# Kernel optimization log

Measured on AMD Instinct MI355X. Metric: run time of the kernel, lower is better.

Reference implementation:

```python
import jax, jax.numpy as jnp
import numpy as np

N0, N1, N2 = 200000, 50000, 10000
D_IN, D_PROMPT, D_HID, D_OUT = 128, 64, 256, 2
E0, E1 = 800000, 160000


def _glorot(key, shape):
    fan_in, fan_out = shape[0], shape[1]
    lim = np.sqrt(6.0 / (fan_in + fan_out))
    return jax.random.uniform(key, shape, jnp.float32, -lim, lim)


def setup_inputs() -> dict:
    key = jax.random.key(0)
    ks = jax.random.split(key, 20)
    inp = {
        "features": jax.random.normal(ks[0], (N0, D_IN), jnp.float32),
        "membership_mask": jax.random.randint(ks[1], (N0,), 0, 2) > 0,
        "src0": jax.random.randint(ks[2], (E0,), 0, N0),
        "dst0": jax.random.randint(ks[3], (E0,), 0, N1),
        "src1": jax.random.randint(ks[4], (E1,), 0, N1),
        "dst1": jax.random.randint(ks[5], (E1,), 0, N2),
        "output_nodes_indices": jax.random.randint(ks[6], (N2,), 0, N2),
        # prompt MLPs
        "w_pin": _glorot(ks[7], (D_IN, D_PROMPT)),
        "b_pin": jnp.zeros((D_PROMPT,), jnp.float32),
        "w_pout": _glorot(ks[8], (D_IN, D_PROMPT)),
        "b_pout": jnp.zeros((D_PROMPT,), jnp.float32),
        # SAGEConv layer 0: (D_IN+D_PROMPT) -> D_HID
        "w_self0": _glorot(ks[9], (D_IN + D_PROMPT, D_HID)),
        "w_neigh0": _glorot(ks[10], (D_IN + D_PROMPT, D_HID)),
        "b0": jnp.zeros((D_HID,), jnp.float32),
        # SAGEConv layer 1: D_HID -> D_HID
        "w_self1": _glorot(ks[11], (D_HID, D_HID)),
        "w_neigh1": _glorot(ks[12], (D_HID, D_HID)),
        "b1": jnp.zeros((D_HID,), jnp.float32),
        # classifier
        "w_cls": _glorot(ks[13], (D_HID, D_OUT)),
        "b_cls": jnp.zeros((D_OUT,), jnp.float32),
    }
    return inp


def _sage_mean(h, src, dst, n_dst, w_self, w_neigh, b):
    # mean-aggregate src features into dst buckets (zero-degree -> 0, DGL semantics)
    agg = jax.ops.segment_sum(h[src], dst, num_segments=n_dst)
    deg = jax.ops.segment_sum(jnp.ones((src.shape[0],), h.dtype), dst, num_segments=n_dst)
    agg = agg / jnp.maximum(deg, 1.0)[:, None]
    return h[:n_dst] @ w_self + agg @ w_neigh + b


def reference(features, membership_mask, src0, dst0, src1, dst1, output_nodes_indices,
              w_pin, b_pin, w_pout, b_pout,
              w_self0, w_neigh0, b0, w_self1, w_neigh1, b1, w_cls, b_cls):
    p_in = jax.nn.relu(features @ w_pin + b_pin)
    p_out = jax.nn.relu(features @ w_pout + b_pout)
    sel = jnp.where(membership_mask[:, None], p_in, p_out)
    h = jnp.concatenate([features, sel], axis=1)          # [N0, D_IN+D_PROMPT]
    h = jax.nn.relu(_sage_mean(h, src0, dst0, N1, w_self0, w_neigh0, b0))  # [N1, D_HID]
    h = _sage_mean(h, src1, dst1, N2, w_self1, w_neigh1, b1)               # [N2, D_HID]
    logits = h @ w_cls + b_cls                             # [N2, D_OUT]
    return logits
```

## Files before the change

### kernel.cpp

```cpp
#include <hip/hip_runtime.h>


#define N0v 200000
#define N1v 50000
#define N2v 10000
#define E0v 800000
#define E1v 160000
#define TB0 49
#define TB1 10
#define TBL (TB0 + TB1)

using u16 = unsigned short;
typedef __attribute__((ext_vector_type(8))) short short8;
typedef __attribute__((ext_vector_type(4))) float f32x4;

__device__ __forceinline__ float b2f(u16 u) {
    union { unsigned int i; float f; } v; v.i = ((unsigned int)u) << 16; return v.f;
}
__device__ __forceinline__ u16 f2b(float f) {
    union { float f; unsigned int i; } v; v.f = f;
    return (u16)((v.i + 0x7fffu + ((v.i >> 16) & 1u)) >> 16);
}
__device__ __forceinline__ void split2(float f, u16& h, u16& l) {
    h = f2b(f);
    l = f2b(f - b2f(h));
}

__global__ void k_prep(const unsigned* mask, int* flag,
                       const float* w_pin, const float* w_pout, u16* WTph, u16* WTpl,
                       const float* ws0, const float* wn0, u16* WT0h, u16* WT0l,
                       const float* ws1, const float* wn1, u16* WT1h, u16* WT1l,
                       const float* bc, float* outp,
                       const int* __restrict__ dst0, const int* __restrict__ dst1,
                       int* cnt0, int* cnt1) {
    const int R0 = 50000;
    const int R1 = R0 + 128 * 128;
    const int R2 = R1 + 256 * 384;
    const int R3 = R2 + 256 * 512;
    const int R4 = R3 + 2 * N2v;
    const int R5 = R4 + E0v;
    const int R6 = R5 + E1v;
    for (int i = blockIdx.x * blockDim.x + threadIdx.x; i < R6;
         i += gridDim.x * blockDim.x) {
        if (i < R0) {
            if (mask[i] > 1u) atomicOr(flag, 1);
        } else if (i < R1) {
            int j = i - R0, n = j >> 7, k = j & 127;
            float f = (n < 64) ? w_pin[k * 64 + n] : w_pout[k * 64 + (n - 64)];
            split2(f, WTph[j], WTpl[j]);
        } else if (i < R2) {
            int j = i - R1, n = j / 384, k = j % 384;
            float f = (k < 192) ? ws0[k * 256 + n] : wn0[(k - 192) * 256 + n];
            split2(f, WT0h[j], WT0l[j]);
        } else if (i < R3) {
            int j = i - R2, n = j >> 9, k = j & 511;
            float f = (k < 256) ? ws1[k * 256 + n] : wn1[(k - 256) * 256 + n];
            split2(f, WT1h[j], WT1l[j]);
        } else if (i < R4) {
            int j = i - R3;
            outp[j] = bc[j & 1];
        } else if (i < R5) {
            atomicAdd(&cnt0[dst0[i - R4]], 1);
        } else {
            atomicAdd(&cnt1[dst1[i - R5]], 1);
        }
    }
}

__global__ __launch_bounds__(256) void k_scan_a(const int* __restrict__ cnt0,
                                                int* __restrict__ off0,
                                                const int* __restrict__ cnt1,
                                                int* __restrict__ off1,
                                                int* __restrict__ tsum) {
    __shared__ int sd[256];
    const int t = threadIdx.x;
    const int blk = blockIdx.x;
    const int g1 = (blk >= TB0);
    const int b = g1 ? blk - TB0 : blk;
    const int n = g1 ? N2v : N1v;
    const int* cnt = g1 ? cnt1 : cnt0;
    int* off = g1 ? off1 : off0;
    const int i0 = b * 1024 + t * 4;
    int c[4] = {0, 0, 0, 0};
    if (i0 + 3 < n) {
        *(int4*)c = *(const int4*)&cnt[i0];
    } else {
        for (int j = 0; j < 4; j++) if (i0 + j < n) c[j] = cnt[i0 + j];
    }
    int s = c[0] + c[1] + c[2] + c[3];
    sd[t] = s;
    __syncthreads();
#pragma unroll
    for (int d = 1; d < 256; d <<= 1) {
        int v = (t >= d) ? sd[t - d] : 0;
        __syncthreads();
        sd[t] += v;
        __syncthreads();
    }
    int run = sd[t] - s;
    int o4[4];
#pragma unroll
    for (int j = 0; j < 4; j++) { o4[j] = run; run += c[j]; }
    if (i0 + 3 < n) *(int4*)&off[i0] = *(const int4*)o4;
    else for (int j = 0; j < 4; j++) if (i0 + j < n) off[i0 + j] = o4[j];
    if (t == 255) tsum[blk] = sd[255];
}

__global__ __launch_bounds__(256) void k_scan_c(int* __restrict__ off0,
                                                int* __restrict__ off1,
                                                const int* __restrict__ tsum) {
    __shared__ int lbase;
    const int t = threadIdx.x;
    const int blk = blockIdx.x;
    const int g1 = (blk >= TB0);
    const int b = g1 ? blk - TB0 : blk;
    const int n = g1 ? N2v : N1v;
    int* off = g1 ? off1 : off0;
    if (t < 64) {
        int v = (t < TBL) ? tsum[t] : 0;
        int incl = v;
#pragma unroll
        for (int d = 1; d < 64; d <<= 1) {
            int u = __shfl_up(incl, d);
            if (t >= d) incl += u;
        }
        int total0 = __shfl(incl, TB0 - 1);
        if (t == blk) lbase = (incl - v) - (g1 ? total0 : 0);
    }
    __syncthreads();
    const int base = lbase;
    const int i0 = b * 1024 + t * 4;
    if (i0 + 3 < n) {
        int4 v = *(int4*)&off[i0];
        v.x += base; v.y += base; v.z += base; v.w += base;
        *(int4*)&off[i0] = v;
    } else {
        for (int j = 0; j < 4; j++) if (i0 + j < n) off[i0 + j] += base;
    }
    if (blk == 0 && t == 0) { off0[N1v] = E0v; off1[N2v] = E1v; }
}

__global__ void k_scatter2(const int* __restrict__ src0, const int* __restrict__ dst0,
                           const int* __restrict__ off0, int* cur0, int* ei0,
                           const int* __restrict__ src1, const int* __restrict__ dst1,
                           const int* __restrict__ off1, int* cur1, int* ei1) {
    for (int i = blockIdx.x * blockDim.x + threadIdx.x; i < E0v + E1v;
         i += gridDim.x * blockDim.x) {
        if (i < E0v) {
            int d = dst0[i];
            ei0[off0[d] + atomicAdd(&cur0[d], 1)] = src0[i];
        } else {
            int d = dst1[i - E0v];
            ei1[off1[d] + atomicAdd(&cur1[d], 1)] = src1[i - E0v];
        }
    }
}

__global__ __launch_bounds__(256, 3) void k_gemm_p(
    const float* __restrict__ A, const u16* __restrict__ Bh, const u16* __restrict__ Bl,
    const float* __restrict__ b_pin, const float* __restrict__ b_pout,
    const void* maskp, const int* __restrict__ flag, u16* __restrict__ G) {
    __shared__ __align__(16) u16 LA[8704];
    const int t = threadIdx.x;
    const int bm = blockIdx.x;
    const int lane = t & 63, w = t >> 6;
    const int m = lane & 15, q = lane >> 4;
    const int r0 = bm * 64;
    const int colbase = w * 32;

    short8 bf[2][4][2];
#pragma unroll
    for (int nt = 0; nt < 2; nt++)
#pragma unroll
        for (int k0 = 0; k0 < 4; k0++) {
            size_t b = (size_t)(colbase + nt * 16 + m) * 128 + k0 * 32 + q * 8;
            bf[nt][k0][0] = *(const short8*)&Bh[b];
            bf[nt][k0][1] = *(const short8*)&Bl[b];
        }

    {
        const int r15 = t >> 4, ch = t & 15;
        const int k0 = ch >> 2, q2 = ch & 3;
#pragma unroll
        for (int p = 0; p < 4; p++) {
            const int row = r0 + r15 + 16 * p;
            const float* ap = &A[(size_t)row * 128 + ch * 8];
            float4 v0 = *(const float4*)ap, v1 = *(const float4*)(ap + 4);
            u16 h8[8];
            h8[0] = f2b(v0.x); h8[1] = f2b(v0.y); h8[2] = f2b(v0.z); h8[3] = f2b(v0.w);
            h8[4] = f2b(v1.x); h8[5] = f2b(v1.y); h8[6] = f2b(v1.z); h8[7] = f2b(v1.w);
            *(uint4*)&G[(size_t)row * 192 + ch * 8] = *(const uint4*)h8;
            *(uint4*)&LA[((p * 4 + k0) * 66 + 16 * q2 + r15) * 8] = *(const uint4*)h8;
        }
    }
    __syncthreads();

    f32x4 acc[4][2] = {};
#pragma unroll
    for (int mi = 0; mi < 4; mi++) {
#pragma unroll
        for (int k0 = 0; k0 < 4; k0++) {
            short8 af = *(const short8*)&LA[((mi * 4 + k0) * 66 + lane) * 8];
#pragma unroll
            for (int nt = 0; nt < 2; nt++) {
                acc[mi][nt] = __builtin_amdgcn_mfma_f32_16x16x32_bf16(af, bf[nt][k0][0], acc[mi][nt], 0, 0, 0);
                acc[mi][nt] = __builtin_amdgcn_mfma_f32_16x16x32_bf16(af, bf[nt][k0][1], acc[mi][nt], 0, 0, 0);
            }
        }
    }

    float bv[2];
#pragma unroll
    for (int nt = 0; nt < 2; nt++) {
        int col = colbase + nt * 16 + m;
        bv[nt] = (col < 64) ? b_pin[col] : b_pout[col - 64];
    }
    __syncthreads();
#pragma unroll
    for (int mi = 0; mi < 4; mi++)
#pragma unroll
        for (int nt = 0; nt < 2; nt++)
#pragma unroll
            for (int r = 0; r < 4; r++) {
                float v = acc[mi][nt][r] + bv[nt];
                v = v > 0.f ? v : 0.f;
                LA[(mi * 16 + q * 4 + r) * 136 + colbase + nt * 16 + m] = f2b(v);
            }
    __syncthreads();
    const int fl = *flag;
    {
        const int c8 = t & 7;
#pragma unroll
        for (int pass = 0; pass < 2; pass++) {
            const int rt = pass * 32 + (t >> 3);
            const int row = r0 + rt;
            bool mk = fl ? (((const unsigned char*)maskp)[row] != 0)
                         : (((const int*)maskp)[row] != 0);
            const int src = mk ? 0 : 64;
            *(uint4*)&G[(size_t)row * 192 + 128 + c8 * 8] =
                *(const uint4*)&LA[rt * 136 + src + c8 * 8];
        }
    }
}

template <int MODE, int KT, int KE0, int MT>
__global__ __launch_bounds__(256, 3) void k_g(
    const u16* __restrict__ A0, int s0, const u16* __restrict__ A1, int s1,
    const u16* __restrict__ Bh, const u16* __restrict__ Bl,
    const float* __restrict__ bias,
    u16* __restrict__ CH, float* __restrict__ outp, const float* __restrict__ wc,
    int M) {
    constexpr int MI = MT / 16;
    __shared__ __align__(16) u16 LA[MI * KT * 66 * 8];
    const int t = threadIdx.x;
    const int bm = blockIdx.x >> 1, bn = blockIdx.x & 1;
    const int lane = t & 63, w = t >> 6;
    const int m = lane & 15, q = lane >> 4;
    const int r0 = bm * MT;
    const int colbase = bn * 128 + w * 32;
    const int K = KT * 32;

    {
        constexpr int TPR = 256 / MT;
        constexpr int SPT = KT / TPR;
        const int rr = t / TPR, sub = t & (TPR - 1);
        int arow = r0 + rr; if (arow >= M) arow = M - 1;
        const int mi = rr >> 4, r15 = rr & 15;
#pragma unroll
        for (int s = 0; s < SPT; s++) {
            const int kc = sub * SPT + s;
#pragma unroll
            for (int q2 = 0; q2 < 4; q2++) {
                const int c = kc * 32 + q2 * 8;
                uint4 v = (c < KE0 * 32)
                              ? *(const uint4*)&A0[(size_t)arow * s0 + c]
                              : *(const uint4*)&A1[(size_t)arow * s1 + (c - KE0 * 32)];
                *(uint4*)&LA[((mi * KT + kc) * 66 + 16 * q2 + r15) * 8] = v;
            }
        }
    }
    __syncthreads();

    f32x4 acc[MI][2] = {};
#pragma unroll 1
    for (int kb = 0; kb < KT; kb += 4) {
        short8 bf[2][4][2];
#pragma unroll
        for (int nt = 0; nt < 2; nt++)
#pragma unroll
            for (int k0 = 0; k0 < 4; k0++) {
                size_t b = (size_t)(colbase + nt * 16 + m) * K + (kb + k0) * 32 + q * 8;
                bf[nt][k0][0] = *(const short8*)&Bh[b];
                bf[nt][k0][1] = *(const short8*)&Bl[b];
            }
#pragma unroll
        for (int mi = 0; mi < MI; mi++) {
#pragma unroll
            for (int k0 = 0; k0 < 4; k0++) {
                short8 af = *(const short8*)&LA[((mi * KT + kb + k0) * 66 + lane) * 8];
#pragma unroll
                for (int nt = 0; nt < 2; nt++) {
                    acc[mi][nt] = __builtin_amdgcn_mfma_f32_16x16x32_bf16(af, bf[nt][k0][0], acc[mi][nt], 0, 0, 0);
                    acc[mi][nt] = __builtin_amdgcn_mfma_f32_16x16x32_bf16(af, bf[nt][k0][1], acc[mi][nt], 0, 0, 0);
                }
            }
        }
    }

    if (MODE == 1) {
        float bv[2];
#pragma unroll
        for (int nt = 0; nt < 2; nt++) bv[nt] = bias[colbase + nt * 16 + m];
        __syncthreads();
#pragma unroll
        for (int mi = 0; mi < MI; mi++)
#pragma unroll
            for (int nt = 0; nt < 2; nt++)
#pragma unroll
                for (int r = 0; r < 4; r++) {
                    float v = acc[mi][nt][r] + bv[nt];
                    v = v > 0.f ? v : 0.f;
                    LA[(mi * 16 + q * 4 + r) * 136 + w * 32 + nt * 16 + m] = f2b(v);
                }
        __syncthreads();
        const int c16 = t & 15;
#pragma unroll
        for (int pass = 0; pass < MT / 16; pass++) {
            const int rt = pass * 16 + (t >> 4);
            const int row = r0 + rt;
            if (row < M) {
                *(uint4*)&CH[(size_t)row * 256 + bn * 128 + c16 * 8] =
                    *(const uint4*)&LA[rt * 136 + c16 * 8];
            }
        }
    } else {
        const int ca = colbase + m, cb = colbase + 16 + m;
        const float bva = bias[ca], bvb = bias[cb];
        const float w0a = wc[ca * 2], w1a = wc[ca * 2 + 1];
        const float w0b = wc[cb * 2], w1b = wc[cb * 2 + 1];
#pragma unroll
        for (int mi = 0; mi < MI; mi++) {
#pragma unroll
            for (int r = 0; r < 4; r++) {
                int row = r0 + mi * 16 + q * 4 + r;
                float va = acc[mi][0][r] + bva;
                float vb = acc[mi][1][r] + bvb;
                float p0 = va * w0a + vb * w0b;
                float p1 = va * w1a + vb * w1b;
#pragma unroll
                for (int s = 1; s < 16; s <<= 1) {
                    p0 += __shfl_xor(p0, s);
                    p1 += __shfl_xor(p1, s);
                }
                if (m == 0 && row < M) {
                    atomicAdd(&outp[row * 2], p0);
                    atomicAdd(&outp[row * 2 + 1], p1);
                }
            }
        }
    }
}

__global__ void k_agg0(const u16* __restrict__ G, const int* __restrict__ off,
                       const int* __restrict__ eidx, u16* __restrict__ aggH) {
    int wid = (blockIdx.x * blockDim.x + threadIdx.x) >> 6;
    int lane = threadIdx.x & 63;
    if (wid >= N1v) return;
    int b = off[wid], e = off[wid + 1];
    float f0 = 0.f, f1 = 0.f, p0 = 0.f;
    for (int base = b; base < e; base += 64) {
        int li = base + lane;
        int idx = eidx[li < e ? li : (e - 1)];
        int nch = e - base; if (nch > 64) nch = 64;
        int j = 0;
        for (; j + 4 <= nch; j += 4) {
            int sa = __shfl(idx, j), sb = __shfl(idx, j + 1);
            int sc = __shfl(idx, j + 2), sd = __shfl(idx, j + 3);
            const u16* ra = &G[(size_t)sa * 192];
            const u16* rb = &G[(size_t)sb * 192];
            const u16* rc = &G[(size_t)sc * 192];
            const u16* rd = &G[(size_t)sd * 192];
            unsigned fa = *(const unsigned*)&ra[2 * lane];
            unsigned fb = *(const unsigned*)&rb[2 * lane];
            unsigned fc = *(const unsigned*)&rc[2 * lane];
            unsigned fd = *(const unsigned*)&rd[2 * lane];
            u16 pa = ra[128 + lane], pb = rb[128 + lane];
            u16 pc = rc[128 + lane], pd = rd[128 + lane];
            f0 += b2f((u16)fa) + b2f((u16)fb) + b2f((u16)fc) + b2f((u16)fd);
            f1 += b2f((u16)(fa >> 16)) + b2f((u16)(fb >> 16)) +
                  b2f((u16)(fc >> 16)) + b2f((u16)(fd >> 16));
            p0 += b2f(pa) + b2f(pb) + b2f(pc) + b2f(pd);
        }
        for (; j < nch; j++) {
            int s = __shfl(idx, j);
            const u16* row = &G[(size_t)s * 192];
            unsigned fv = *(const unsigned*)&row[2 * lane];
            f0 += b2f((u16)fv);
            f1 += b2f((u16)(fv >> 16));
            p0 += b2f(row[128 + lane]);
        }
    }
    int deg = e - b;
    float inv = 1.0f / (float)(deg > 1 ? deg : 1);
    size_t rb2 = (size_t)wid * 192;
    *(unsigned*)&aggH[rb2 + 2 * lane] =
        (unsigned)f2b(f0 * inv) | ((unsigned)f2b(f1 * inv) << 16);
    aggH[rb2 + 128 + lane] = f2b(p0 * inv);
}

__global__ void k_agg1(const u16* __restrict__ h1H, const int* __restrict__ off,
                       const int* __restrict__ eidx, u16* __restrict__ aggH) {
    int wid = (blockIdx.x * blockDim.x + threadIdx.x) >> 6;
    int lane = threadIdx.x & 63;
    if (wid >= N2v) return;
    int b = off[wid], e = off[wid + 1];
    float a0 = 0.f, a1 = 0.f, a2 = 0.f, a3 = 0.f;
    for (int base = b; base < e; base += 64) {
        int li = base + lane;
        int idx = eidx[li < e ? li : (e - 1)];
        int nch = e - base; if (nch > 64) nch = 64;
        int j = 0;
        for (; j + 4 <= nch; j += 4) {
            int sa = __shfl(idx, j), sb = __shfl(idx, j + 1);
            int sc = __shfl(idx, j + 2), sd = __shfl(idx, j + 3);
            const u16* ra = &h1H[(size_t)sa * 256];
            const u16* rb = &h1H[(size_t)sb * 256];
            const u16* rc = &h1H[(size_t)sc * 256];
            const u16* rd = &h1H[(size_t)sd * 256];
            unsigned va0 = *(const unsigned*)&ra[2 * lane];
            unsigned vb0 = *(const unsigned*)&rb[2 * lane];
            unsigned vc0 = *(const unsigned*)&rc[2 * lane];
            unsigned vd0 = *(const unsigned*)&rd[2 * lane];
            unsigned va1 = *(const unsigned*)&ra[128 + 2 * lane];
            unsigned vb1 = *(const unsigned*)&rb[128 + 2 * lane];
            unsigned vc1 = *(const unsigned*)&rc[128 + 2 * lane];
            unsigned vd1 = *(const unsigned*)&rd[128 + 2 * lane];
            a0 += b2f((u16)va0) + b2f((u16)vb0) + b2f((u16)vc0) + b2f((u16)vd0);
            a1 += b2f((u16)(va0 >> 16)) + b2f((u16)(vb0 >> 16)) +
                  b2f((u16)(vc0 >> 16)) + b2f((u16)(vd0 >> 16));
            a2 += b2f((u16)va1) + b2f((u16)vb1) + b2f((u16)vc1) + b2f((u16)vd1);
            a3 += b2f((u16)(va1 >> 16)) + b2f((u16)(vb1 >> 16)) +
                  b2f((u16)(vc1 >> 16)) + b2f((u16)(vd1 >> 16));
        }
        for (; j < nch; j++) {
            int s = __shfl(idx, j);
            const u16* row = &h1H[(size_t)s * 256];
            unsigned v0 = *(const unsigned*)&row[2 * lane];
            unsigned v1 = *(const unsigned*)&row[128 + 2 * lane];
            a0 += b2f((u16)v0); a1 += b2f((u16)(v0 >> 16));
            a2 += b2f((u16)v1); a3 += b2f((u16)(v1 >> 16));
        }
    }
    int deg = e - b;
    float inv = 1.0f / (float)(deg > 1 ? deg : 1);
    size_t rb2 = (size_t)wid * 256;
    *(unsigned*)&aggH[rb2 + 2 * lane] =
        (unsigned)f2b(a0 * inv) | ((unsigned)f2b(a1 * inv) << 16);
    *(unsigned*)&aggH[rb2 + 128 + 2 * lane] =
        (unsigned)f2b(a2 * inv) | ((unsigned)f2b(a3 * inv) << 16);
}

extern "C" void kernel_launch(void* const* d_in, const int* in_sizes, int n_in,
                              void* d_out, int out_size, void* d_ws, size_t ws_size,
                              hipStream_t stream) {
    const float* features = (const float*)d_in[0];
    const void* maskp     = d_in[1];
    const int* src0       = (const int*)d_in[2];
    const int* dst0       = (const int*)d_in[3];
    const int* src1       = (const int*)d_in[4];
    const int* dst1       = (const int*)d_in[5];
    const float* w_pin    = (const float*)d_in[7];
    const float* b_pin    = (const float*)d_in[8];
    const float* w_pout   = (const float*)d_in[9];
    const float* b_pout   = (const float*)d_in[10];
    const float* w_self0  = (const float*)d_in[11];
    const float* w_neigh0 = (const float*)d_in[12];
    const float* b0       = (const float*)d_in[13];
    const float* w_self1  = (const float*)d_in[14];
    const float* w_neigh1 = (const float*)d_in[15];
    const float* b1       = (const float*)d_in[16];
    const float* w_cls    = (const float*)d_in[17];
    const float* b_cls    = (const float*)d_in[18];
    float* out = (float*)d_out;
    (void)in_sizes; (void)n_in; (void)out_size; (void)ws_size;

    char* ws = (char*)d_ws;
    size_t o = 0;
    auto alloc = [&](size_t bytes) { size_t r = o; o += (bytes + 255) & ~(size_t)255; return r; };
    size_t o_flag = alloc(4);
    size_t o_cnt0 = alloc(N1v * 4);
    size_t o_cur0 = alloc(N1v * 4);
    size_t o_cnt1 = alloc(N2v * 4);
    size_t o_cur1 = alloc(N2v * 4);
    size_t zero_end = o;
    size_t o_G    = alloc((size_t)N0v * 192 * 2);
    size_t o_aggH = alloc((size_t)N1v * 192 * 2);
    size_t o_h1H  = alloc((size_t)N1v * 256 * 2);
    size_t o_ag1H = alloc((size_t)N2v * 256 * 2);
    size_t o_wtph = alloc(128 * 128 * 2), o_wtpl = alloc(128 * 128 * 2);
    size_t o_wt0h = alloc(256 * 384 * 2), o_wt0l = alloc(256 * 384 * 2);
    size_t o_wt1h = alloc(256 * 512 * 2), o_wt1l = alloc(256 * 512 * 2);
    size_t o_off0 = alloc((N1v + 1) * 4);
    size_t o_off1 = alloc((N2v + 1) * 4);
    size_t o_ei0  = alloc((size_t)E0v * 4);
    size_t o_ei1  = alloc((size_t)E1v * 4);
    size_t o_tsum = alloc(TBL * 4);

    int* flag = (int*)(ws + o_flag);
    int* cnt0 = (int*)(ws + o_cnt0);
    int* cur0 = (int*)(ws + o_cur0);
    int* cnt1 = (int*)(ws + o_cnt1);
    int* cur1 = (int*)(ws + o_cur1);
    u16* G     = (u16*)(ws + o_G);
    u16* aggH  = (u16*)(ws + o_aggH);
    u16* h1H   = (u16*)(ws + o_h1H);
    u16* ag1H  = (u16*)(ws + o_ag1H);
    u16* WTph = (u16*)(ws + o_wtph);
    u16* WTpl = (u16*)(ws + o_wtpl);
    u16* WT0h = (u16*)(ws + o_wt0h);
    u16* WT0l = (u16*)(ws + o_wt0l);
    u16* WT1h = (u16*)(ws + o_wt1h);
    u16* WT1l = (u16*)(ws + o_wt1l);
    int* off0 = (int*)(ws + o_off0);
    int* off1 = (int*)(ws + o_off1);
    int* ei0  = (int*)(ws + o_ei0);
    int* ei1  = (int*)(ws + o_ei1);
    int* tsum = (int*)(ws + o_tsum);

    hipMemsetAsync(ws + o_flag, 0, zero_end - o_flag, stream);

    k_prep<<<1024, 256, 0, stream>>>((const unsigned*)maskp, flag,
                                     w_pin, w_pout, WTph, WTpl,
                                     w_self0, w_neigh0, WT0h, WT0l,
                                     w_self1, w_neigh1, WT1h, WT1l,
                                     b_cls, out, dst0, dst1, cnt0, cnt1);

    k_scan_a<<<TBL, 256, 0, stream>>>(cnt0, off0, cnt1, off1, tsum);
    k_scan_c<<<TBL, 256, 0, stream>>>(off0, off1, tsum);

    k_scatter2<<<1024, 256, 0, stream>>>(src0, dst0, off0, cur0, ei0,
                                         src1, dst1, off1, cur1, ei1);

    k_gemm_p<<<N0v / 64, 256, 0, stream>>>(features, WTph, WTpl,
                                           b_pin, b_pout, maskp, flag, G);

    k_agg0<<<(N1v + 3) / 4, 256, 0, stream>>>(G, off0, ei0, aggH);

    k_g<1, 12, 6, 64><<<((N1v + 63) / 64) * 2, 256, 0, stream>>>(
        G, 192, aggH, 192, WT0h, WT0l, b0, h1H, nullptr, nullptr, N1v);

    k_agg1<<<(N2v + 3) / 4, 256, 0, stream>>>(h1H, off1, ei1, ag1H);

    k_g<3, 16, 8, 32><<<((N2v + 31) / 32) * 2, 256, 0, stream>>>(
        h1H, 256, ag1H, 256, WT1h, WT1l, b1, nullptr, out, w_cls, N2v);
}
```

Measured before the change: 445.2 us.

## Record edge ranks during counting, partition scatter, and stream B fragments in GEMMs

The counting pass now stores the return value of each atomicAdd as the edge's rank within its destination bucket. The scatter uses that rank directly instead of a second round of atomics on cursor arrays. The scatter also splits its grid into 8 destination partitions, so each block re-reads its edge chunk but only writes edges whose destination falls in its partition, to localise writes. Both GEMM kernels load B fragments one k-step at a time (prefetched in k_gemm_p) instead of holding all of them in registers, mask loads are hoisted, and k_gemm_p's launch-bounds occupancy goes from 3 to 4; the cost is extra rank buffers and redundant index reads in the scatter.

Measured after the change: 422.0 us. 1.05x faster.

```diff
diff --git a/kernel.cpp b/kernel.cpp
--- a/kernel.cpp
+++ b/kernel.cpp
@@ -32,7 +32,7 @@
                        const float* ws1, const float* wn1, u16* WT1h, u16* WT1l,
                        const float* bc, float* outp,
                        const int* __restrict__ dst0, const int* __restrict__ dst1,
-                       int* cnt0, int* cnt1) {
+                       int* cnt0, int* cnt1, int* rk0, int* rk1) {
     const int R0 = 50000;
     const int R1 = R0 + 128 * 128;
     const int R2 = R1 + 256 * 384;
@@ -60,9 +60,11 @@
             int j = i - R3;
             outp[j] = bc[j & 1];
         } else if (i < R5) {
-            atomicAdd(&cnt0[dst0[i - R4]], 1);
+            int e = i - R4;
+            rk0[e] = atomicAdd(&cnt0[dst0[e]], 1);
         } else {
-            atomicAdd(&cnt1[dst1[i - R5]], 1);
+            int e = i - R5;
+            rk1[e] = atomicAdd(&cnt1[dst1[e]], 1);
         }
     }
 }
@@ -140,23 +142,33 @@
     if (blk == 0 && t == 0) { off0[N1v] = E0v; off1[N2v] = E1v; }
 }
 
-__global__ void k_scatter2(const int* __restrict__ src0, const int* __restrict__ dst0,
-                           const int* __restrict__ off0, int* cur0, int* ei0,
-                           const int* __restrict__ src1, const int* __restrict__ dst1,
-                           const int* __restrict__ off1, int* cur1, int* ei1) {
-    for (int i = blockIdx.x * blockDim.x + threadIdx.x; i < E0v + E1v;
-         i += gridDim.x * blockDim.x) {
-        if (i < E0v) {
+__global__ __launch_bounds__(256) void k_scatter2(
+    const int* __restrict__ src0, const int* __restrict__ dst0,
+    const int* __restrict__ off0, const int* __restrict__ rk0, int* __restrict__ ei0,
+    const int* __restrict__ src1, const int* __restrict__ dst1,
+    const int* __restrict__ off1, const int* __restrict__ rk1, int* __restrict__ ei1) {
+    const int part = blockIdx.x & 7;
+    const int chunk = blockIdx.x >> 3;
+    const int nch = gridDim.x >> 3;
+    {
+        const int per = (E0v + nch - 1) / nch;
+        const int i1 = min((chunk + 1) * per, E0v);
+        for (int i = chunk * per + (int)threadIdx.x; i < i1; i += 256) {
             int d = dst0[i];
-            ei0[off0[d] + atomicAdd(&cur0[d], 1)] = src0[i];
-        } else {
-            int d = dst1[i - E0v];
-            ei1[off1[d] + atomicAdd(&cur1[d], 1)] = src1[i - E0v];
-        }
-    }
-}
-
-__global__ __launch_bounds__(256, 3) void k_gemm_p(
+            if (d / 6250 == part) ei0[off0[d] + rk0[i]] = src0[i];
+        }
+    }
+    {
+        const int per = (E1v + nch - 1) / nch;
+        const int i1 = min((chunk + 1) * per, E1v);
+        for (int i = chunk * per + (int)threadIdx.x; i < i1; i += 256) {
+            int d = dst1[i];
+            if (d / 1250 == part) ei1[off1[d] + rk1[i]] = src1[i];
+        }
+    }
+}
+
+__global__ __launch_bounds__(256, 4) void k_gemm_p(
     const float* __restrict__ A, const u16* __restrict__ Bh, const u16* __restrict__ Bl,
     const float* __restrict__ b_pin, const float* __restrict__ b_pout,
     const void* maskp, const int* __restrict__ flag, u16* __restrict__ G) {
@@ -168,15 +180,25 @@
     const int r0 = bm * 64;
     const int colbase = w * 32;
 
-    short8 bf[2][4][2];
-#pragma unroll
-    for (int nt = 0; nt < 2; nt++)
-#pragma unroll
-        for (int k0 = 0; k0 < 4; k0++) {
-            size_t b = (size_t)(colbase + nt * 16 + m) * 128 + k0 * 32 + q * 8;
-            bf[nt][k0][0] = *(const short8*)&Bh[b];
-            bf[nt][k0][1] = *(const short8*)&Bl[b];
-        }
+    const int fl = *flag;
+    bool mk0, mk1;
+    {
+        const int ra = r0 + (t >> 3), rb = ra + 32;
+        if (fl) {
+            mk0 = ((const unsigned char*)maskp)[ra] != 0;
+            mk1 = ((const unsigned char*)maskp)[rb] != 0;
+        } else {
+            mk0 = ((const int*)maskp)[ra] != 0;
+            mk1 = ((const int*)maskp)[rb] != 0;
+        }
+    }
+
+    const size_t ba = (size_t)(colbase + m) * 128 + q * 8;
+    const size_t bb = (size_t)(colbase + 16 + m) * 128 + q * 8;
+    short8 nb0h = *(const short8*)&Bh[ba];
+    short8 nb0l = *(const short8*)&Bl[ba];
+    short8 nb1h = *(const short8*)&Bh[bb];
+    short8 nb1l = *(const short8*)&Bl[bb];
 
     {
         const int r15 = t >> 4, ch = t & 15;
@@ -197,15 +219,21 @@
 
     f32x4 acc[4][2] = {};
 #pragma unroll
-    for (int mi = 0; mi < 4; mi++) {
-#pragma unroll
-        for (int k0 = 0; k0 < 4; k0++) {
+    for (int k0 = 0; k0 < 4; k0++) {
+        short8 b0h = nb0h, b0l = nb0l, b1h = nb1h, b1l = nb1l;
+        if (k0 < 3) {
+            nb0h = *(const short8*)&Bh[ba + (k0 + 1) * 32];
+            nb0l = *(const short8*)&Bl[ba + (k0 + 1) * 32];
+            nb1h = *(const short8*)&Bh[bb + (k0 + 1) * 32];
+            nb1l = *(const short8*)&Bl[bb + (k0 + 1) * 32];
+        }
+#pragma unroll
+        for (int mi = 0; mi < 4; mi++) {
             short8 af = *(const short8*)&LA[((mi * 4 + k0) * 66 + lane) * 8];
-#pragma unroll
-            for (int nt = 0; nt < 2; nt++) {
-                acc[mi][nt] = __builtin_amdgcn_mfma_f32_16x16x32_bf16(af, bf[nt][k0][0], acc[mi][nt], 0, 0, 0);
-                acc[mi][nt] = __builtin_amdgcn_mfma_f32_16x16x32_bf16(af, bf[nt][k0][1], acc[mi][nt], 0, 0, 0);
-            }
+            acc[mi][0] = __builtin_amdgcn_mfma_f32_16x16x32_bf16(af, b0h, acc[mi][0], 0, 0, 0);
+            acc[mi][0] = __builtin_amdgcn_mfma_f32_16x16x32_bf16(af, b0l, acc[mi][0], 0, 0, 0);
+            acc[mi][1] = __builtin_amdgcn_mfma_f32_16x16x32_bf16(af, b1h, acc[mi][1], 0, 0, 0);
+            acc[mi][1] = __builtin_amdgcn_mfma_f32_16x16x32_bf16(af, b1l, acc[mi][1], 0, 0, 0);
         }
     }
 
@@ -227,19 +255,13 @@
                 LA[(mi * 16 + q * 4 + r) * 136 + colbase + nt * 16 + m] = f2b(v);
             }
     __syncthreads();
-    const int fl = *flag;
     {
         const int c8 = t & 7;
-#pragma unroll
-        for (int pass = 0; pass < 2; pass++) {
-            const int rt = pass * 32 + (t >> 3);
-            const int row = r0 + rt;
-            bool mk = fl ? (((const unsigned char*)maskp)[row] != 0)
-                         : (((const int*)maskp)[row] != 0);
-            const int src = mk ? 0 : 64;
-            *(uint4*)&G[(size_t)row * 192 + 128 + c8 * 8] =
-                *(const uint4*)&LA[rt * 136 + src + c8 * 8];
-        }
+        const int rt = t >> 3;
+        *(uint4*)&G[(size_t)(r0 + rt) * 192 + 128 + c8 * 8] =
+            *(const uint4*)&LA[rt * 136 + (mk0 ? 0 : 64) + c8 * 8];
+        *(uint4*)&G[(size_t)(r0 + 32 + rt) * 192 + 128 + c8 * 8] =
+            *(const uint4*)&LA[(32 + rt) * 136 + (mk1 ? 0 : 64) + c8 * 8];
     }
 }
 
@@ -281,28 +303,26 @@
     }
     __syncthreads();
 
+    const size_t ba = (size_t)(colbase + m) * K + q * 8;
+    const size_t bb = (size_t)(colbase + 16 + m) * K + q * 8;
+
     f32x4 acc[MI][2] = {};
 #pragma unroll 1
     for (int kb = 0; kb < KT; kb += 4) {
-        short8 bf[2][4][2];
-#pragma unroll
-        for (int nt = 0; nt < 2; nt++)
-#pragma unroll
-            for (int k0 = 0; k0 < 4; k0++) {
-                size_t b = (size_t)(colbase + nt * 16 + m) * K + (kb + k0) * 32 + q * 8;
-                bf[nt][k0][0] = *(const short8*)&Bh[b];
-                bf[nt][k0][1] = *(const short8*)&Bl[b];
-            }
-#pragma unroll
-        for (int mi = 0; mi < MI; mi++) {
-#pragma unroll
-            for (int k0 = 0; k0 < 4; k0++) {
+#pragma unroll
+        for (int k0 = 0; k0 < 4; k0++) {
+            const size_t ko = (size_t)(kb + k0) * 32;
+            short8 b0h = *(const short8*)&Bh[ba + ko];
+            short8 b0l = *(const short8*)&Bl[ba + ko];
+            short8 b1h = *(const short8*)&Bh[bb + ko];
+            short8 b1l = *(const short8*)&Bl[bb + ko];
+#pragma unroll
+            for (int mi = 0; mi < MI; mi++) {
                 short8 af = *(const short8*)&LA[((mi * KT + kb + k0) * 66 + lane) * 8];
-#pragma unroll
-                for (int nt = 0; nt < 2; nt++) {
-                    acc[mi][nt] = __builtin_amdgcn_mfma_f32_16x16x32_bf16(af, bf[nt][k0][0], acc[mi][nt], 0, 0, 0);
-                    acc[mi][nt] = __builtin_amdgcn_mfma_f32_16x16x32_bf16(af, bf[nt][k0][1], acc[mi][nt], 0, 0, 0);
-                }
+                acc[mi][0] = __builtin_amdgcn_mfma_f32_16x16x32_bf16(af, b0h, acc[mi][0], 0, 0, 0);
+                acc[mi][0] = __builtin_amdgcn_mfma_f32_16x16x32_bf16(af, b0l, acc[mi][0], 0, 0, 0);
+                acc[mi][1] = __builtin_amdgcn_mfma_f32_16x16x32_bf16(af, b1h, acc[mi][1], 0, 0, 0);
+                acc[mi][1] = __builtin_amdgcn_mfma_f32_16x16x32_bf16(af, b1l, acc[mi][1], 0, 0, 0);
             }
         }
     }
@@ -489,9 +509,7 @@
     auto alloc = [&](size_t bytes) { size_t r = o; o += (bytes + 255) & ~(size_t)255; return r; };
     size_t o_flag = alloc(4);
     size_t o_cnt0 = alloc(N1v * 4);
-    size_t o_cur0 = alloc(N1v * 4);
     size_t o_cnt1 = alloc(N2v * 4);
-    size_t o_cur1 = alloc(N2v * 4);
     size_t zero_end = o;
     size_t o_G    = alloc((size_t)N0v * 192 * 2);
     size_t o_aggH = alloc((size_t)N1v * 192 * 2);
@@ -504,13 +522,13 @@
     size_t o_off1 = alloc((N2v + 1) * 4);
     size_t o_ei0  = alloc((size_t)E0v * 4);
     size_t o_ei1  = alloc((size_t)E1v * 4);
+    size_t o_rk0  = alloc((size_t)E0v * 4);
+    size_t o_rk1  = alloc((size_t)E1v * 4);
     size_t o_tsum = alloc(TBL * 4);
 
     int* flag = (int*)(ws + o_flag);
     int* cnt0 = (int*)(ws + o_cnt0);
-    int* cur0 = (int*)(ws + o_cur0);
     int* cnt1 = (int*)(ws + o_cnt1);
-    int* cur1 = (int*)(ws + o_cur1);
     u16* G     = (u16*)(ws + o_G);
     u16* aggH  = (u16*)(ws + o_aggH);
     u16* h1H   = (u16*)(ws + o_h1H);
@@ -525,6 +543,8 @@
     int* off1 = (int*)(ws + o_off1);
     int* ei0  = (int*)(ws + o_ei0);
     int* ei1  = (int*)(ws + o_ei1);
+    int* rk0  = (int*)(ws + o_rk0);
+    int* rk1  = (int*)(ws + o_rk1);
     int* tsum = (int*)(ws + o_tsum);
 
     hipMemsetAsync(ws + o_flag, 0, zero_end - o_flag, stream);
@@ -533,13 +553,13 @@
                                      w_pin, w_pout, WTph, WTpl,
                                      w_self0, w_neigh0, WT0h, WT0l,
                                      w_self1, w_neigh1, WT1h, WT1l,
-                                     b_cls, out, dst0, dst1, cnt0, cnt1);
+                                     b_cls, out, dst0, dst1, cnt0, cnt1, rk0, rk1);
 
     k_scan_a<<<TBL, 256, 0, stream>>>(cnt0, off0, cnt1, off1, tsum);
     k_scan_c<<<TBL, 256, 0, stream>>>(off0, off1, tsum);
 
-    k_scatter2<<<1024, 256, 0, stream>>>(src0, dst0, off0, cur0, ei0,
-                                         src1, dst1, off1, cur1, ei1);
+    k_scatter2<<<2048, 256, 0, stream>>>(src0, dst0, off0, rk0, ei0,
+                                         src1, dst1, off1, rk1, ei1);
 
     k_gemm_p<<<N0v / 64, 256, 0, stream>>>(features, WTph, WTpl,
                                            b_pin, b_pout, maskp, flag, G);
```
